# Optimization experiments

Hardware: AMD Instinct MI355X
Metric: run time of the kernel (lower is better)

The kernel has to match this reference:

```python
import jax, jax.numpy as jnp
import numpy as np

NUM_ENT, SEQ, H, OUT, NG = 10000, 10, 200, 100, 2048


def _seg_mean(x, idx, n):
    s = jax.ops.segment_sum(x, idx, num_segments=n)
    d = jax.ops.segment_sum(jnp.ones((idx.shape[0],), x.dtype), idx, num_segments=n)
    return s / jnp.maximum(d, 1.0)[:, None]


def setup_inputs() -> dict:
    k = jax.random.split(jax.random.key(0), 24)
    N, E, Nw, Ew, Vw, Rsel, MQ = 50000, 200000, 30000, 300000, 40000, 8192, 8
    f = lambda i, shp: jax.random.normal(k[i], shp, jnp.float32) * 0.05
    ri = lambda i, shp, hi: jax.random.randint(k[i], shp, 0, hi)
    return dict(
        ent_embeds=f(0, (NUM_ENT, H)), rel_embeds=f(1, (240, H)), word_embeds=f(2, (Vw, OUT)),
        gcn_w1=f(3, (OUT, H)), gcn_b1=jnp.zeros((H,), jnp.float32),
        gcn_w2=f(4, (H, H)), gcn_b2=jnp.zeros((H,), jnp.float32),
        cg1_wn=f(5, (H, OUT)), cg1_wl=f(6, (H, OUT)), cg1_wr=f(7, (H, OUT)),
        cg2_wn=f(8, (OUT, H)), cg2_wl=f(9, (OUT, H)), cg2_wr=f(10, (OUT, H)),
        attn_wa=f(11, (H, H)), attn_wc=f(12, (2 * H, H)),
        node_slot=jnp.arange(N), edge_src=ri(13, (E,), N), edge_dst=ri(14, (E,), N),
        edge_type=ri(15, (E,), 240), word_id=ri(16, (Nw,), Vw),
        wsrc=ri(17, (Ew,), Nw), wdst=ri(18, (Ew,), Nw),
        ent_word_idx=ri(19, (N, MQ), Nw), ent_word_mask=ri(20, (N, MQ), 2).astype(jnp.int32),
        rel_word_idx=ri(21, (Rsel, MQ), Nw), rel_word_mask=ri(22, (Rsel, MQ), 2).astype(jnp.int32),
        r_ids_graph=ri(23, (Rsel,), E), edge_slot=jnp.arange(Rsel))


def reference(ent_embeds, rel_embeds, word_embeds, gcn_w1, gcn_b1, gcn_w2, gcn_b2,
              cg1_wn, cg1_wl, cg1_wr, cg2_wn, cg2_wl, cg2_wr, attn_wa, attn_wc,
              node_slot, edge_src, edge_dst, edge_type, word_id, wsrc, wdst,
              ent_word_idx, ent_word_mask, rel_word_idx, rel_word_mask, r_ids_graph, edge_slot):
    N = node_slot.shape[0]
    Nw = word_id.shape[0]
    Rsel = r_ids_graph.shape[0]
    # --- se_aggr: 2-layer GCN over the batched word graph ---
    wh = word_embeds[word_id]                                   # [Nw,100]
    wh = jax.nn.relu(_seg_mean(wh[wsrc], wdst, Nw) @ gcn_w1 + gcn_b1)
    wh = jax.nn.relu(_seg_mean(wh[wsrc], wdst, Nw) @ gcn_w2 + gcn_b2)
    # --- re_aggr1/re_aggr2: CompGCN message passing on batched event graph ---
    h = ent_embeds[node_slot % NUM_ENT]                         # [N,200]
    e = rel_embeds[edge_type]                                   # [E,200]
    def compgcn(h, e, wn, wl, wr):
        agg = _seg_mean(h[edge_src] - e, edge_dst, N)           # sub-composition msgs
        return jax.nn.relu(agg @ wn + h @ wl), e @ wr
    h, e = compgcn(h, e, cg1_wn, cg1_wl, cg1_wr)                # 200 -> 100
    h, e = compgcn(h, e, cg2_wn, cg2_wl, cg2_wr)                # 100 -> 200
    embeds_g_r = e[r_ids_graph]                                 # [Rsel,200]
    # --- build Q_mx / H_mx (padded word-context groups) + 'general' attention ---
    Q = jnp.concatenate([h, embeds_g_r], 0)                     # [N+Rsel,200]
    H_ent = wh[ent_word_idx] * ent_word_mask[..., None].astype(wh.dtype)   # [N,8,200]
    H_rel = wh[rel_word_idx] * rel_word_mask[..., None].astype(wh.dtype)   # [Rsel,8,200]
    Hm = jnp.concatenate([H_ent, H_rel], 0)                     # [N+Rsel,8,200]
    scores = jnp.einsum('md,de,mke->mk', Q, attn_wa, Hm)
    attn = jax.nn.softmax(scores, axis=-1)
    ctx = jnp.einsum('mk,mkd->md', attn, Hm)
    out = jnp.tanh(jnp.concatenate([ctx, Q], -1) @ attn_wc)     # [N+Rsel,200]
    h_out, r_out = out[:N], out[N:]
    # --- temporal scatter of node embeddings per snapshot graph ---
    nid = node_slot % NUM_ENT
    gidx = node_slot // (N // SEQ)
    node_emb_temporal = jnp.zeros((NUM_ENT, SEQ, H), h_out.dtype).at[nid, gidx].set(h_out)
    # --- pack selected edge embeds into padded [NG, SEQ, H] sequence tensor ---
    per = Rsel // NG
    row, pos = edge_slot // per, edge_slot % per
    embed_seq = jnp.zeros((NG, SEQ, H), r_out.dtype).at[row, pos].set(r_out)
    return embed_seq, node_emb_temporal
```

## Files before the change

kernel.cpp:

```cpp
#include <hip/hip_runtime.h>
#include <cstddef>

constexpr int NUM_ENT_C = 10000;
constexpr int SEQ_C     = 10;
constexpr int H_C       = 200;
constexpr int OUT_C     = 100;
constexpr int NG_C      = 2048;
constexpr int NREL_C    = 240;
constexpr int MQ_C      = 8;

typedef __attribute__((ext_vector_type(8))) short          bf16x8;
typedef __attribute__((ext_vector_type(4))) float          f32x4;
typedef __attribute__((ext_vector_type(8))) unsigned short u16x8;

__device__ __forceinline__ unsigned short f2bf(float v) {
    unsigned u = __float_as_uint(v);
    unsigned r = (u + 0x7FFFu + ((u >> 16) & 1u)) >> 16;
    return (unsigned short)r;
}
__device__ __forceinline__ float bf2f(unsigned short b) {
    return __uint_as_float((unsigned)b << 16);
}
__device__ __forceinline__ void up2(unsigned u, float& lo, float& hi) {
    lo = __uint_as_float(u << 16);
    hi = __uint_as_float(u & 0xFFFF0000u);
}

__global__ void prep_k(const float* __restrict__ ent, unsigned short* __restrict__ entb, size_t e8,
                       const float* __restrict__ wemb, unsigned short* __restrict__ wembb, size_t w8,
                       int* __restrict__ wdeg, int Nw, int* __restrict__ edeg, int N) {
    size_t total = e8 + w8 + (size_t)Nw + (size_t)N;
    size_t stride = (size_t)gridDim.x * blockDim.x;
    for (size_t t = (size_t)blockIdx.x * blockDim.x + threadIdx.x; t < total; t += stride) {
        if (t < e8) {
            const float* s = ent + t * 8;
            u16x8 o;
            #pragma unroll
            for (int i = 0; i < 8; ++i) o[i] = f2bf(s[i]);
            *reinterpret_cast<u16x8*>(entb + t * 8) = o;
        } else if (t < e8 + w8) {
            size_t tt = t - e8;
            const float* s = wemb + tt * 8;
            u16x8 o;
            #pragma unroll
            for (int i = 0; i < 8; ++i) o[i] = f2bf(s[i]);
            *reinterpret_cast<u16x8*>(wembb + tt * 8) = o;
        } else if (t < e8 + w8 + (size_t)Nw) {
            wdeg[t - e8 - w8] = 0;
        } else {
            edeg[t - e8 - w8 - Nw] = 0;
        }
    }
}

__global__ void hist2_k(const int* __restrict__ wdst, int Ew, int* __restrict__ wdeg,
                        const int* __restrict__ edst, int E, int* __restrict__ edeg) {
    int total = Ew + E;
    int stride = gridDim.x * blockDim.x;
    for (int t = blockIdx.x * blockDim.x + threadIdx.x; t < total; t += stride) {
        if (t < Ew) atomicAdd(&wdeg[wdst[t]], 1);
        else        atomicAdd(&edeg[edst[t - Ew]], 1);
    }
}

__global__ void scanA_k(const int* __restrict__ v, int* __restrict__ bsum, int n) {
    __shared__ int s[256];
    int t = threadIdx.x;
    int i = blockIdx.x * 256 + t;
    s[t] = (i < n) ? v[i] : 0;
    __syncthreads();
    for (int d = 128; d; d >>= 1) {
        if (t < d) s[t] += s[t + d];
        __syncthreads();
    }
    if (t == 0) bsum[blockIdx.x] = s[0];
}

__global__ void scanB_k(int* __restrict__ bsum, int nb) {
    __shared__ int s[256];
    int t = threadIdx.x;
    int v = (t < nb) ? bsum[t] : 0;
    s[t] = v;
    __syncthreads();
    for (int d = 1; d < 256; d <<= 1) {
        int x = (t >= d) ? s[t - d] : 0;
        __syncthreads();
        s[t] += x;
        __syncthreads();
    }
    if (t < nb) bsum[t] = s[t] - v;
}

__global__ void scanC_k(const int* __restrict__ v, const int* __restrict__ bsum,
                        int* __restrict__ offs, int* __restrict__ cur, int n) {
    __shared__ int s[256];
    int t = threadIdx.x;
    int i = blockIdx.x * 256 + t;
    int val = (i < n) ? v[i] : 0;
    s[t] = val;
    __syncthreads();
    for (int d = 1; d < 256; d <<= 1) {
        int x = (t >= d) ? s[t - d] : 0;
        __syncthreads();
        s[t] += x;
        __syncthreads();
    }
    if (i < n) {
        int ex = s[t] - val + bsum[blockIdx.x];
        offs[i] = ex;
        cur[i]  = ex;
    }
}

__global__ void fill2_k(const int* __restrict__ wdst, const int* __restrict__ wsrc,
                        const int* __restrict__ word_id, int Ew,
                        int* __restrict__ wcur, int* __restrict__ wbktA, int* __restrict__ wbktB,
                        const int* __restrict__ edst, const int* __restrict__ esrc,
                        const int* __restrict__ etype, int E,
                        int* __restrict__ ecur, int* __restrict__ ebktS, int* __restrict__ ebktT) {
    int total = Ew + E;
    int stride = gridDim.x * blockDim.x;
    for (int t = blockIdx.x * blockDim.x + threadIdx.x; t < total; t += stride) {
        if (t < Ew) {
            int ws = wsrc[t];
            int p = atomicAdd(&wcur[wdst[t]], 1);
            wbktA[p] = word_id[ws];
            wbktB[p] = ws;
        } else {
            int e = t - Ew;
            int p = atomicAdd(&ecur[edst[e]], 1);
            ebktS[p] = esrc[e];
            ebktT[p] = etype[e];
        }
    }
}

template<int K1, int K2, int Kp, bool RELSUB, bool SRCMOD, bool SELFMOD, bool DUAL>
__global__ __launch_bounds__(256) void gather_mean_k(
        const unsigned short* __restrict__ feat, const unsigned short* __restrict__ selfT,
        const float* __restrict__ rel,
        const int* __restrict__ bktS, const int* __restrict__ bktT,
        const int* __restrict__ offs, const int* __restrict__ deg,
        unsigned short* __restrict__ dst, int n) {
    int node = blockIdx.x * 4 + (threadIdx.x >> 6);
    int lane = threadIdx.x & 63;
    if (node >= n) return;
    int off = offs[node], dg = deg[node];
    float acc[4] = {0.f, 0.f, 0.f, 0.f};
    unsigned short* drow = dst + (size_t)node * Kp;

    if (DUAL) {
        int half = lane >> 5, lh = lane & 31;
        int d0 = lh * 4;
        bool act = d0 < K1;
        for (int i = 0; i < dg; i += 2) {
            int ii = i + half;
            if (ii < dg && act) {
                int s = bktS[off + ii];
                if (SRCMOD) s = s % NUM_ENT_C;
                uint2 u = *reinterpret_cast<const uint2*>(feat + (size_t)s * K1 + d0);
                float e0, e1, e2, e3;
                up2(u.x, e0, e1); up2(u.y, e2, e3);
                if (RELSUB) {
                    int tt = bktT[off + ii];
                    float4 rv = *reinterpret_cast<const float4*>(rel + (size_t)tt * K1 + d0);
                    e0 -= rv.x; e1 -= rv.y; e2 -= rv.z; e3 -= rv.w;
                }
                acc[0] += e0; acc[1] += e1; acc[2] += e2; acc[3] += e3;
            }
        }
        #pragma unroll
        for (int c = 0; c < 4; ++c) acc[c] += __shfl_xor(acc[c], 32);
        float inv = 1.f / fmaxf((float)dg, 1.f);
        if (half == 0 && act) {
            uint2 o;
            o.x = (unsigned)f2bf(acc[0] * inv) | ((unsigned)f2bf(acc[1] * inv) << 16);
            o.y = (unsigned)f2bf(acc[2] * inv) | ((unsigned)f2bf(acc[3] * inv) << 16);
            *reinterpret_cast<uint2*>(drow + d0) = o;
        }
        if (K2 > 0 && half == 1 && d0 < K2) {
            int srow = SELFMOD ? (node % NUM_ENT_C) : node;
            uint2 sv = *reinterpret_cast<const uint2*>(selfT + (size_t)srow * K2 + d0);
            *reinterpret_cast<uint2*>(drow + K1 + d0) = sv;
        }
    } else {
        int d0 = lane * 4;
        bool act = d0 < K1;
        for (int i = 0; i < dg; ++i) {
            if (act) {
                int s = bktS[off + i];
                if (SRCMOD) s = s % NUM_ENT_C;
                uint2 u = *reinterpret_cast<const uint2*>(feat + (size_t)s * K1 + d0);
                float e0, e1, e2, e3;
                up2(u.x, e0, e1); up2(u.y, e2, e3);
                if (RELSUB) {
                    int tt = bktT[off + i];
                    float4 rv = *reinterpret_cast<const float4*>(rel + (size_t)tt * K1 + d0);
                    e0 -= rv.x; e1 -= rv.y; e2 -= rv.z; e3 -= rv.w;
                }
                acc[0] += e0; acc[1] += e1; acc[2] += e2; acc[3] += e3;
            }
        }
        float inv = 1.f / fmaxf((float)dg, 1.f);
        if (act) {
            uint2 o;
            o.x = (unsigned)f2bf(acc[0] * inv) | ((unsigned)f2bf(acc[1] * inv) << 16);
            o.y = (unsigned)f2bf(acc[2] * inv) | ((unsigned)f2bf(acc[3] * inv) << 16);
            *reinterpret_cast<uint2*>(drow + d0) = o;
        }
        if (K2 > 0 && d0 < K2) {
            int srow = SELFMOD ? (node % NUM_ENT_C) : node;
            uint2 sv = *reinterpret_cast<const uint2*>(selfT + (size_t)srow * K2 + d0);
            *reinterpret_cast<uint2*>(drow + K1 + d0) = sv;
        }
    }
    for (int cc = K1 + K2 + lane; cc < Kp; cc += 64) drow[cc] = 0;
}

__global__ void convw_all_k(const float* __restrict__ gcn_w1, const float* __restrict__ gcn_w2,
                            const float* __restrict__ cg1_wn, const float* __restrict__ cg1_wl,
                            const float* __restrict__ cg2_wn, const float* __restrict__ cg2_wl,
                            const float* __restrict__ attn_wa, const float* __restrict__ attn_wc,
                            unsigned short* __restrict__ Wt) {
    constexpr int S0 = 26624;
    constexpr int S1 = S0 + 46592;
    constexpr int S2 = S1 + 46592;
    constexpr int S3 = S2 + 46592;
    constexpr int S4 = S3 + 46592;
    constexpr int S5 = S4 + 86528;
    int stride = gridDim.x * blockDim.x;
    for (int t = blockIdx.x * blockDim.x + threadIdx.x; t < S5; t += stride) {
        float v = 0.f;
        if (t < S0) {
            int l = t, nn = l >> 7, k = l & 127;
            if (nn < 200 && k < 100) v = gcn_w1[k * 200 + nn];
        } else if (t < S1) {
            int l = t - S0, nn = l / 224, k = l - nn * 224;
            if (nn < 200 && k < 200) v = gcn_w2[k * 200 + nn];
        } else if (t < S2) {
            int l = t - S1, nn = l / 416, k = l - nn * 416;
            if (nn < 100) {
                if (k < 200)      v = cg1_wn[k * 100 + nn];
                else if (k < 400) v = cg1_wl[(k - 200) * 100 + nn];
            }
        } else if (t < S3) {
            int l = t - S2, nn = l / 224, k = l - nn * 224;
            if (nn < 200) {
                if (k < 100)      v = cg2_wn[k * 200 + nn];
                else if (k < 200) v = cg2_wl[(k - 100) * 200 + nn];
            }
        } else if (t < S4) {
            int l = t - S3, nn = l / 224, k = l - nn * 224;
            if (nn < 200 && k < 200) v = attn_wa[k * 200 + nn];
        } else {
            int l = t - S4, nn = l / 416, k = l - nn * 416;
            if (nn < 200 && k < 400) v = attn_wc[k * 200 + nn];
        }
        Wt[t] = f2bf(v);
    }
}

__global__ void post_k(const float* __restrict__ rel2, const int* __restrict__ edge_type,
                       const int* __restrict__ r_ids, unsigned short* __restrict__ A,
                       const int* __restrict__ node_slot, const int* __restrict__ edge_slot,
                       int* __restrict__ rowOff, int N, int M, int divq, int per, int embBase) {
    int R = M - N;
    size_t secA = (size_t)R * H_C;
    size_t secB = secA + (size_t)M * 6;
    size_t total = secB + (size_t)M;
    size_t stride = (size_t)gridDim.x * blockDim.x;
    for (size_t t = (size_t)blockIdx.x * blockDim.x + threadIdx.x; t < total; t += stride) {
        if (t < secA) {
            int r = (int)(t / H_C);
            int d = (int)(t - (size_t)r * H_C);
            int rr = r_ids[r];
            A[(size_t)(N + r) * 448 + 200 + d] = f2bf(rel2[(size_t)edge_type[rr] * H_C + d]);
        } else if (t < secB) {
            size_t l = t - secA;
            int m = (int)(l / 6), c = (int)(l - (size_t)m * 6);
            *reinterpret_cast<uint4*>(A + (size_t)m * 448 + 400 + c * 8) = make_uint4(0u, 0u, 0u, 0u);
        } else {
            int m = (int)(t - secB);
            int offv;
            if (m < N) {
                int ns = node_slot[m];
                offv = embBase + ((ns % NUM_ENT_C) * SEQ_C + ns / divq) * H_C;
            } else {
                int es = edge_slot[m - N];
                offv = ((es / per) * SEQ_C + (es - (es / per) * per)) * H_C;
            }
            rowOff[m] = offv;
        }
    }
}

template<int NF, int ACT, bool SCATTER, bool OBF16>
__global__ __launch_bounds__(256) void mfma_gemm_k(
        const unsigned short* __restrict__ A, int lda,
        const unsigned short* __restrict__ Wt,
        const float* __restrict__ bias, void* __restrict__ Cv, int ldc,
        const int* __restrict__ rowOff, int M, int N, int Kp) {
    constexpr int BN = NF * 16;
    __shared__ unsigned short As[128][40];
    __shared__ unsigned short Bs[BN][40];
    const int tid  = threadIdx.x;
    const int bm   = blockIdx.x * 128;
    const int w    = tid >> 6;
    const int lane = tid & 63;
    const int lr   = lane & 15;
    const int lk   = (lane >> 4) * 8;

    f32x4 acc0[NF], acc1[NF];
    #pragma unroll
    for (int nf = 0; nf < NF; ++nf) {
        acc0[nf] = (f32x4){0.f, 0.f, 0.f, 0.f};
        acc1[nf] = (f32x4){0.f, 0.f, 0.f, 0.f};
    }

    for (int k0 = 0; k0 < Kp; k0 += 32) {
        #pragma unroll
        for (int j = 0; j < 2; ++j) {
            int id = tid + j * 256;
            int m = id >> 2, c = id & 3;
            int gm = bm + m;
            uint4 v = make_uint4(0u, 0u, 0u, 0u);
            if (gm < M) v = *reinterpret_cast<const uint4*>(A + (size_t)gm * lda + k0 + c * 8);
            *reinterpret_cast<uint4*>(&As[m][c * 8]) = v;
        }
        for (int i = tid; i < NF * 64; i += 256) {
            int n = i >> 2, c = i & 3;
            uint4 v = *reinterpret_cast<const uint4*>(Wt + (size_t)n * Kp + k0 + c * 8);
            *reinterpret_cast<uint4*>(&Bs[n][c * 8]) = v;
        }
        __syncthreads();
        bf16x8 a0 = *reinterpret_cast<const bf16x8*>(&As[w * 16 + lr][lk]);
        bf16x8 a1 = *reinterpret_cast<const bf16x8*>(&As[64 + w * 16 + lr][lk]);
        #pragma unroll
        for (int nf = 0; nf < NF; ++nf) {
            bf16x8 b = *reinterpret_cast<const bf16x8*>(&Bs[nf * 16 + lr][lk]);
            acc0[nf] = __builtin_amdgcn_mfma_f32_16x16x32_bf16(a0, b, acc0[nf], 0, 0, 0);
            acc1[nf] = __builtin_amdgcn_mfma_f32_16x16x32_bf16(a1, b, acc1[nf], 0, 0, 0);
        }
        __syncthreads();
    }

    const int r0 = (lane >> 4) * 4;
    #pragma unroll
    for (int h = 0; h < 2; ++h) {
        #pragma unroll
        for (int j = 0; j < 4; ++j) {
            int gm = bm + h * 64 + w * 16 + r0 + j;
            if (gm >= M) continue;
            size_t base;
            if (SCATTER && !OBF16) base = (size_t)rowOff[gm];
            else                   base = (size_t)gm * ldc;
            #pragma unroll
            for (int nf = 0; nf < NF; ++nf) {
                int gn = nf * 16 + lr;
                if (gn >= N) continue;
                float v = h ? acc1[nf][j] : acc0[nf][j];
                if (bias) v += bias[gn];
                if (ACT == 1) v = fmaxf(v, 0.f);
                if (ACT == 2) v = tanhf(v);
                if (OBF16) ((unsigned short*)Cv)[base + gn] = f2bf(v);
                else       ((float*)Cv)[base + gn] = v;
            }
        }
    }
}

template<int NF, int ACT, bool SCATTER, bool OBF16>
static void launch_mfma(hipStream_t s, const unsigned short* A, int lda,
                        const unsigned short* Wt, const float* bias,
                        void* C, int ldc, const int* rowOff, int M, int N, int Kp) {
    mfma_gemm_k<NF, ACT, SCATTER, OBF16><<<dim3((M + 127) / 128), 256, 0, s>>>(
        A, lda, Wt, bias, C, ldc, rowOff, M, N, Kp);
}

__global__ __launch_bounds__(256) void gemm_f32_k(
        const float* __restrict__ A, const float* __restrict__ W,
        float* __restrict__ C, int M, int N, int K) {
    constexpr int TS = 64, BK = 16;
    __shared__ float As[BK][TS];
    __shared__ float Bs[BK][TS];
    int bm = blockIdx.x * TS, bn = blockIdx.y * TS;
    int tid = threadIdx.x;
    int tx = tid & 15, ty = tid >> 4;
    float acc[4][4] = {};
    for (int k0 = 0; k0 < K; k0 += BK) {
        #pragma unroll
        for (int l = tid; l < TS * BK; l += 256) {
            int m = l >> 4, kk = l & 15;
            int gm = bm + m, gk = k0 + kk;
            As[kk][m] = (gm < M && gk < K) ? A[(size_t)gm * K + gk] : 0.f;
        }
        #pragma unroll
        for (int l = tid; l < TS * BK; l += 256) {
            int kk = l >> 6, n = l & 63;
            int gk = k0 + kk, gn = bn + n;
            Bs[kk][n] = (gk < K && gn < N) ? W[(size_t)gk * N + gn] : 0.f;
        }
        __syncthreads();
        #pragma unroll
        for (int kk = 0; kk < BK; ++kk) {
            float a[4], b[4];
            #pragma unroll
            for (int i = 0; i < 4; ++i) a[i] = As[kk][ty * 4 + i];
            #pragma unroll
            for (int j = 0; j < 4; ++j) b[j] = Bs[kk][tx * 4 + j];
            #pragma unroll
            for (int i = 0; i < 4; ++i)
                #pragma unroll
                for (int j = 0; j < 4; ++j) acc[i][j] += a[i] * b[j];
        }
        __syncthreads();
    }
    #pragma unroll
    for (int i = 0; i < 4; ++i) {
        int gm = bm + ty * 4 + i;
        if (gm >= M) continue;
        #pragma unroll
        for (int j = 0; j < 4; ++j) {
            int gn = bn + tx * 4 + j;
            if (gn < N) C[(size_t)gm * N + gn] = acc[i][j];
        }
    }
}

__global__ __launch_bounds__(256) void attn_k(
        const unsigned short* __restrict__ QAb, const unsigned short* __restrict__ whb,
        const int* __restrict__ ent_idx, const int* __restrict__ ent_mask,
        const int* __restrict__ rel_idx, const int* __restrict__ rel_mask,
        unsigned short* __restrict__ ctxOut, int N, int M) {
    int m = blockIdx.x * 4 + (threadIdx.x >> 6);
    int lane = threadIdx.x & 63;
    if (m >= M) return;
    const int* idxp;
    const int* mskp;
    if (m < N) { idxp = ent_idx + (size_t)m * MQ_C;        mskp = ent_mask + (size_t)m * MQ_C; }
    else       { idxp = rel_idx + (size_t)(m - N) * MQ_C;  mskp = rel_mask + (size_t)(m - N) * MQ_C; }

    int d0 = lane * 4;
    bool act = d0 < H_C;
    float qa0 = 0.f, qa1 = 0.f, qa2 = 0.f, qa3 = 0.f;
    if (act) {
        uint2 u = *reinterpret_cast<const uint2*>(QAb + (size_t)m * H_C + d0);
        up2(u.x, qa0, qa1); up2(u.y, qa2, qa3);
    }
    int   idx[MQ_C];
    float msk[MQ_C];
    float s[MQ_C];
    uint2 wr[MQ_C];
    #pragma unroll
    for (int k = 0; k < MQ_C; ++k) { idx[k] = idxp[k]; msk[k] = (float)mskp[k]; }
    #pragma unroll
    for (int k = 0; k < MQ_C; ++k) {
        float p = 0.f;
        if (act) {
            wr[k] = *reinterpret_cast<const uint2*>(whb + (size_t)idx[k] * H_C + d0);
            float e0, e1, e2, e3;
            up2(wr[k].x, e0, e1); up2(wr[k].y, e2, e3);
            p = qa0 * e0 + qa1 * e1 + qa2 * e2 + qa3 * e3;
        } else {
            wr[k] = make_uint2(0u, 0u);
        }
        #pragma unroll
        for (int off = 32; off; off >>= 1) p += __shfl_xor(p, off);
        s[k] = p * msk[k];
    }
    float mx = s[0];
    #pragma unroll
    for (int k = 1; k < MQ_C; ++k) mx = fmaxf(mx, s[k]);
    float den = 0.f;
    #pragma unroll
    for (int k = 0; k < MQ_C; ++k) { s[k] = expf(s[k] - mx); den += s[k]; }
    float inv = 1.f / den;
    if (act) {
        float c0 = 0.f, c1 = 0.f, c2 = 0.f, c3 = 0.f;
        #pragma unroll
        for (int k = 0; k < MQ_C; ++k) {
            float a = s[k] * msk[k];
            float e0, e1, e2, e3;
            up2(wr[k].x, e0, e1); up2(wr[k].y, e2, e3);
            c0 += a * e0; c1 += a * e1; c2 += a * e2; c3 += a * e3;
        }
        uint2 o;
        o.x = (unsigned)f2bf(c0 * inv) | ((unsigned)f2bf(c1 * inv) << 16);
        o.y = (unsigned)f2bf(c2 * inv) | ((unsigned)f2bf(c3 * inv) << 16);
        *reinterpret_cast<uint2*>(ctxOut + (size_t)m * 448 + d0) = o;
    }
}


static inline dim3 ew_grid(size_t total) {
    size_t b = (total + 255) / 256;
    if (b > 4096) b = 4096;
    return dim3((unsigned)b);
}

extern "C" void kernel_launch(void* const* d_in, const int* in_sizes, int n_in,
                              void* d_out, int out_size, void* d_ws, size_t ws_size,
                              hipStream_t stream) {
    const float* ent_embeds = (const float*)d_in[0];
    const float* rel_embeds = (const float*)d_in[1];
    const float* word_embeds= (const float*)d_in[2];
    const float* gcn_w1     = (const float*)d_in[3];
    const float* gcn_b1     = (const float*)d_in[4];
    const float* gcn_w2     = (const float*)d_in[5];
    const float* gcn_b2     = (const float*)d_in[6];
    const float* cg1_wn     = (const float*)d_in[7];
    const float* cg1_wl     = (const float*)d_in[8];
    const float* cg1_wr     = (const float*)d_in[9];
    const float* cg2_wn     = (const float*)d_in[10];
    const float* cg2_wl     = (const float*)d_in[11];
    const float* cg2_wr     = (const float*)d_in[12];
    const float* attn_wa    = (const float*)d_in[13];
    const float* attn_wc    = (const float*)d_in[14];
    const int* node_slot    = (const int*)d_in[15];
    const int* edge_src     = (const int*)d_in[16];
    const int* edge_dst     = (const int*)d_in[17];
    const int* edge_type    = (const int*)d_in[18];
    const int* word_id      = (const int*)d_in[19];
    const int* wsrc         = (const int*)d_in[20];
    const int* wdst         = (const int*)d_in[21];
    const int* ent_word_idx = (const int*)d_in[22];
    const int* ent_word_mask= (const int*)d_in[23];
    const int* rel_word_idx = (const int*)d_in[24];
    const int* rel_word_mask= (const int*)d_in[25];
    const int* r_ids_graph  = (const int*)d_in[26];
    const int* edge_slot    = (const int*)d_in[27];

    const int N    = in_sizes[15];
    const int E    = in_sizes[16];
    const int Nw   = in_sizes[19];
    const int Ew   = in_sizes[20];
    const int Rsel = in_sizes[27];
    const int M    = N + Rsel;
    const int divq = N / SEQ_C;
    const int per  = Rsel / NG_C;
    const int embBase = NG_C * SEQ_C * H_C;
    const size_t entElems  = (size_t)in_sizes[0];
    const size_t wembElems = (size_t)in_sizes[2];

    float* ws = (float*)d_ws;
    size_t o = 0;
    auto align4 = [&]() { o = (o + 3) & ~(size_t)3; };
    int* wdeg  = (int*)(ws + o); o += Nw;
    int* woffs = (int*)(ws + o); o += Nw;
    int* wcur  = (int*)(ws + o); o += Nw;
    int* edeg  = (int*)(ws + o); o += N;
    int* eoffs = (int*)(ws + o); o += N;
    int* ecur  = (int*)(ws + o); o += N;
    int* wbktA = (int*)(ws + o); o += Ew;
    int* wbktB = (int*)(ws + o); o += Ew;
    int* ebktS = (int*)(ws + o); o += E;
    int* ebktT = (int*)(ws + o); o += E;
    int* bsum  = (int*)(ws + o); o += 256;
    int* rowOff= (int*)(ws + o); o += M;
    float* rel1 = ws + o; o += (size_t)NREL_C * OUT_C;
    float* rel2 = ws + o; o += (size_t)NREL_C * H_C;
    align4();
    unsigned short* Wt      = (unsigned short*)(ws + o); o += 299520 / 2;
    align4();
    unsigned short* wh_bf   = (unsigned short*)(ws + o); o += ((size_t)Nw * H_C) / 2;
    align4();
    unsigned short* h1_bf   = (unsigned short*)(ws + o); o += ((size_t)N * OUT_C) / 2;
    align4();
    unsigned short* ent_bf  = (unsigned short*)(ws + o); o += entElems / 2;
    align4();
    unsigned short* wemb_bf = (unsigned short*)(ws + o); o += wembElems / 2;
    align4();
    unsigned short* AbfF    = (unsigned short*)(ws + o); o += ((size_t)M * 448) / 2;
    align4();
    float* BIG = ws + o;
    unsigned short* wh1_bf = (unsigned short*)BIG;
    unsigned short* AbfW   = (unsigned short*)(BIG + ((size_t)Nw * H_C) / 2);
    unsigned short* AbfE   = (unsigned short*)BIG;
    unsigned short* QAb    = (unsigned short*)d_out;

    unsigned short* WT_g1 = Wt;
    unsigned short* WT_g2 = Wt + 26624;
    unsigned short* WT_c1 = Wt + 73216;
    unsigned short* WT_c2 = Wt + 119808;
    unsigned short* WT_wa = Wt + 166400;
    unsigned short* WT_wc = Wt + 212992;

    prep_k<<<ew_grid(entElems / 8 + wembElems / 8 + Nw + N), 256, 0, stream>>>(
        ent_embeds, ent_bf, entElems / 8, word_embeds, wemb_bf, wembElems / 8,
        wdeg, Nw, edeg, N);
    convw_all_k<<<ew_grid(299520), 256, 0, stream>>>(
        gcn_w1, gcn_w2, cg1_wn, cg1_wl, cg2_wn, cg2_wl, attn_wa, attn_wc, Wt);
    hist2_k<<<ew_grid((size_t)Ew + E), 256, 0, stream>>>(wdst, Ew, wdeg, edge_dst, E, edeg);
    {
        int nbW = (Nw + 255) / 256;
        scanA_k<<<nbW, 256, 0, stream>>>(wdeg, bsum, Nw);
        scanB_k<<<1, 256, 0, stream>>>(bsum, nbW);
        scanC_k<<<nbW, 256, 0, stream>>>(wdeg, bsum, woffs, wcur, Nw);
        int nbE = (N + 255) / 256;
        scanA_k<<<nbE, 256, 0, stream>>>(edeg, bsum, N);
        scanB_k<<<1, 256, 0, stream>>>(bsum, nbE);
        scanC_k<<<nbE, 256, 0, stream>>>(edeg, bsum, eoffs, ecur, N);
    }
    fill2_k<<<ew_grid((size_t)Ew + E), 256, 0, stream>>>(
        wdst, wsrc, word_id, Ew, wcur, wbktA, wbktB,
        edge_dst, edge_src, edge_type, E, ecur, ebktS, ebktT);
    gemm_f32_k<<<dim3((NREL_C + 63) / 64, (OUT_C + 63) / 64), 256, 0, stream>>>(
        rel_embeds, cg1_wr, rel1, NREL_C, OUT_C, H_C);
    gemm_f32_k<<<dim3((NREL_C + 63) / 64, (H_C + 63) / 64), 256, 0, stream>>>(
        rel1, cg2_wr, rel2, NREL_C, H_C, OUT_C);
    post_k<<<ew_grid((size_t)Rsel * H_C + (size_t)M * 7), 256, 0, stream>>>(
        rel2, edge_type, r_ids_graph, AbfF, node_slot, edge_slot, rowOff,
        N, M, divq, per, embBase);

    gather_mean_k<OUT_C, 0, 128, false, false, false, true><<<dim3((Nw + 3) / 4), 256, 0, stream>>>(
        wemb_bf, nullptr, nullptr, wbktA, nullptr, woffs, wdeg, AbfW, Nw);
    launch_mfma<13, 1, false, true>(stream, AbfW, 128, WT_g1, gcn_b1, wh1_bf, H_C, nullptr, Nw, H_C, 128);
    gather_mean_k<H_C, 0, 224, false, false, false, false><<<dim3((Nw + 3) / 4), 256, 0, stream>>>(
        wh1_bf, nullptr, nullptr, wbktB, nullptr, woffs, wdeg, AbfW, Nw);
    launch_mfma<13, 1, false, true>(stream, AbfW, 224, WT_g2, gcn_b2, wh_bf, H_C, nullptr, Nw, H_C, 224);

    gather_mean_k<H_C, H_C, 448, true, true, true, false><<<dim3((N + 3) / 4), 256, 0, stream>>>(
        ent_bf, ent_bf, rel_embeds, ebktS, ebktT, eoffs, edeg, AbfE, N);
    launch_mfma<7, 1, false, true>(stream, AbfE, 448, WT_c1, nullptr, h1_bf, OUT_C, nullptr, N, OUT_C, 416);
    gather_mean_k<OUT_C, OUT_C, 224, true, false, false, true><<<dim3((N + 3) / 4), 256, 0, stream>>>(
        h1_bf, h1_bf, rel1, ebktS, ebktT, eoffs, edeg, AbfE, N);
    launch_mfma<13, 1, false, true>(stream, AbfE, 224, WT_c2, nullptr, AbfF + 200, 448, nullptr, N, H_C, 224);

    launch_mfma<13, 0, false, true>(stream, AbfF + 200, 448, WT_wa, nullptr, QAb, H_C, nullptr, M, H_C, 224);
    attn_k<<<(M + 3) / 4, 256, 0, stream>>>(QAb, wh_bf, ent_word_idx, ent_word_mask,
                                            rel_word_idx, rel_word_mask, AbfF, N, M);
    hipMemsetAsync(d_out, 0, (size_t)out_size * 4, stream);
    launch_mfma<13, 2, true, false>(stream, AbfF, 448, WT_wc, nullptr, d_out, H_C, rowOff, M, H_C, 416);
}
```

Before: 722.9 us.

## Merge word and entity CSR builds into one scan; unroll gathers; skip masked attention loads

The word-graph and event-graph degree arrays and buckets now share one concatenated CSR, so a single three-kernel scan replaces two. This removes three kernel launches and their serialization, and scanB grows to 512 threads to cover the larger block count. The non-dual gather loop is unrolled by two to keep more independent loads in flight. The attention kernel skips loading and reducing word rows whose mask is zero, which saves memory traffic but adds a divergent branch.

```diff
diff --git a/kernel.cpp b/kernel.cpp
--- a/kernel.cpp
+++ b/kernel.cpp
@@ -28,8 +28,8 @@
 
 __global__ void prep_k(const float* __restrict__ ent, unsigned short* __restrict__ entb, size_t e8,
                        const float* __restrict__ wemb, unsigned short* __restrict__ wembb, size_t w8,
-                       int* __restrict__ wdeg, int Nw, int* __restrict__ edeg, int N) {
-    size_t total = e8 + w8 + (size_t)Nw + (size_t)N;
+                       int* __restrict__ cdeg, int nNodes) {
+    size_t total = e8 + w8 + (size_t)nNodes;
     size_t stride = (size_t)gridDim.x * blockDim.x;
     for (size_t t = (size_t)blockIdx.x * blockDim.x + threadIdx.x; t < total; t += stride) {
         if (t < e8) {
@@ -45,21 +45,20 @@
             #pragma unroll
             for (int i = 0; i < 8; ++i) o[i] = f2bf(s[i]);
             *reinterpret_cast<u16x8*>(wembb + tt * 8) = o;
-        } else if (t < e8 + w8 + (size_t)Nw) {
-            wdeg[t - e8 - w8] = 0;
         } else {
-            edeg[t - e8 - w8 - Nw] = 0;
-        }
-    }
-}
-
-__global__ void hist2_k(const int* __restrict__ wdst, int Ew, int* __restrict__ wdeg,
-                        const int* __restrict__ edst, int E, int* __restrict__ edeg) {
+            cdeg[t - e8 - w8] = 0;
+        }
+    }
+}
+
+__global__ void hist2_k(const int* __restrict__ wdst, int Ew,
+                        const int* __restrict__ edst, int E,
+                        int* __restrict__ cdeg, int Nw) {
     int total = Ew + E;
     int stride = gridDim.x * blockDim.x;
     for (int t = blockIdx.x * blockDim.x + threadIdx.x; t < total; t += stride) {
-        if (t < Ew) atomicAdd(&wdeg[wdst[t]], 1);
-        else        atomicAdd(&edeg[edst[t - Ew]], 1);
+        if (t < Ew) atomicAdd(&cdeg[wdst[t]], 1);
+        else        atomicAdd(&cdeg[Nw + edst[t - Ew]], 1);
     }
 }
 
@@ -77,12 +76,12 @@
 }
 
 __global__ void scanB_k(int* __restrict__ bsum, int nb) {
-    __shared__ int s[256];
+    __shared__ int s[512];
     int t = threadIdx.x;
     int v = (t < nb) ? bsum[t] : 0;
     s[t] = v;
     __syncthreads();
-    for (int d = 1; d < 256; d <<= 1) {
+    for (int d = 1; d < 512; d <<= 1) {
         int x = (t >= d) ? s[t - d] : 0;
         __syncthreads();
         s[t] += x;
@@ -114,23 +113,23 @@
 
 __global__ void fill2_k(const int* __restrict__ wdst, const int* __restrict__ wsrc,
                         const int* __restrict__ word_id, int Ew,
-                        int* __restrict__ wcur, int* __restrict__ wbktA, int* __restrict__ wbktB,
                         const int* __restrict__ edst, const int* __restrict__ esrc,
                         const int* __restrict__ etype, int E,
-                        int* __restrict__ ecur, int* __restrict__ ebktS, int* __restrict__ ebktT) {
+                        int* __restrict__ ccur, int Nw,
+                        int* __restrict__ bktA, int* __restrict__ bktB) {
     int total = Ew + E;
     int stride = gridDim.x * blockDim.x;
     for (int t = blockIdx.x * blockDim.x + threadIdx.x; t < total; t += stride) {
         if (t < Ew) {
-            int ws = wsrc[t];
-            int p = atomicAdd(&wcur[wdst[t]], 1);
-            wbktA[p] = word_id[ws];
-            wbktB[p] = ws;
+            int s = wsrc[t];
+            int p = atomicAdd(&ccur[wdst[t]], 1);
+            bktA[p] = word_id[s];
+            bktB[p] = s;
         } else {
             int e = t - Ew;
-            int p = atomicAdd(&ecur[edst[e]], 1);
-            ebktS[p] = esrc[e];
-            ebktT[p] = etype[e];
+            int p = atomicAdd(&ccur[Nw + edst[e]], 1);
+            bktA[p] = esrc[e];
+            bktB[p] = etype[e];
         }
     }
 }
@@ -186,11 +185,31 @@
     } else {
         int d0 = lane * 4;
         bool act = d0 < K1;
-        for (int i = 0; i < dg; ++i) {
+        int i = 0;
+        for (; i + 2 <= dg; i += 2) {
+            int s0 = bktS[off + i], s1 = bktS[off + i + 1];
+            if (SRCMOD) { s0 = s0 % NUM_ENT_C; s1 = s1 % NUM_ENT_C; }
             if (act) {
-                int s = bktS[off + i];
-                if (SRCMOD) s = s % NUM_ENT_C;
-                uint2 u = *reinterpret_cast<const uint2*>(feat + (size_t)s * K1 + d0);
+                uint2 u0 = *reinterpret_cast<const uint2*>(feat + (size_t)s0 * K1 + d0);
+                uint2 u1 = *reinterpret_cast<const uint2*>(feat + (size_t)s1 * K1 + d0);
+                float a0, a1, a2, a3, b0, b1, b2, b3;
+                up2(u0.x, a0, a1); up2(u0.y, a2, a3);
+                up2(u1.x, b0, b1); up2(u1.y, b2, b3);
+                if (RELSUB) {
+                    int t0 = bktT[off + i], t1 = bktT[off + i + 1];
+                    float4 r0 = *reinterpret_cast<const float4*>(rel + (size_t)t0 * K1 + d0);
+                    float4 r1 = *reinterpret_cast<const float4*>(rel + (size_t)t1 * K1 + d0);
+                    a0 -= r0.x; a1 -= r0.y; a2 -= r0.z; a3 -= r0.w;
+                    b0 -= r1.x; b1 -= r1.y; b2 -= r1.z; b3 -= r1.w;
+                }
+                acc[0] += a0 + b0; acc[1] += a1 + b1; acc[2] += a2 + b2; acc[3] += a3 + b3;
+            }
+        }
+        if (i < dg) {
+            int s0 = bktS[off + i];
+            if (SRCMOD) s0 = s0 % NUM_ENT_C;
+            if (act) {
+                uint2 u = *reinterpret_cast<const uint2*>(feat + (size_t)s0 * K1 + d0);
                 float e0, e1, e2, e3;
                 up2(u.x, e0, e1); up2(u.y, e2, e3);
                 if (RELSUB) {
@@ -447,26 +466,31 @@
         uint2 u = *reinterpret_cast<const uint2*>(QAb + (size_t)m * H_C + d0);
         up2(u.x, qa0, qa1); up2(u.y, qa2, qa3);
     }
-    int   idx[MQ_C];
-    float msk[MQ_C];
+    int  idx[MQ_C];
+    int  msk[MQ_C];
     float s[MQ_C];
     uint2 wr[MQ_C];
     #pragma unroll
-    for (int k = 0; k < MQ_C; ++k) { idx[k] = idxp[k]; msk[k] = (float)mskp[k]; }
+    for (int k = 0; k < MQ_C; ++k) { idx[k] = idxp[k]; msk[k] = mskp[k]; }
     #pragma unroll
     for (int k = 0; k < MQ_C; ++k) {
-        float p = 0.f;
-        if (act) {
-            wr[k] = *reinterpret_cast<const uint2*>(whb + (size_t)idx[k] * H_C + d0);
-            float e0, e1, e2, e3;
-            up2(wr[k].x, e0, e1); up2(wr[k].y, e2, e3);
-            p = qa0 * e0 + qa1 * e1 + qa2 * e2 + qa3 * e3;
+        if (msk[k] != 0) {
+            float p = 0.f;
+            if (act) {
+                wr[k] = *reinterpret_cast<const uint2*>(whb + (size_t)idx[k] * H_C + d0);
+                float e0, e1, e2, e3;
+                up2(wr[k].x, e0, e1); up2(wr[k].y, e2, e3);
+                p = qa0 * e0 + qa1 * e1 + qa2 * e2 + qa3 * e3;
+            } else {
+                wr[k] = make_uint2(0u, 0u);
+            }
+            #pragma unroll
+            for (int off = 32; off; off >>= 1) p += __shfl_xor(p, off);
+            s[k] = p;
         } else {
+            s[k] = 0.f;
             wr[k] = make_uint2(0u, 0u);
         }
-        #pragma unroll
-        for (int off = 32; off; off >>= 1) p += __shfl_xor(p, off);
-        s[k] = p * msk[k];
     }
     float mx = s[0];
     #pragma unroll
@@ -479,10 +503,11 @@
         float c0 = 0.f, c1 = 0.f, c2 = 0.f, c3 = 0.f;
         #pragma unroll
         for (int k = 0; k < MQ_C; ++k) {
-            float a = s[k] * msk[k];
-            float e0, e1, e2, e3;
-            up2(wr[k].x, e0, e1); up2(wr[k].y, e2, e3);
-            c0 += a * e0; c1 += a * e1; c2 += a * e2; c3 += a * e3;
+            if (msk[k] != 0) {
+                float e0, e1, e2, e3;
+                up2(wr[k].x, e0, e1); up2(wr[k].y, e2, e3);
+                c0 += s[k] * e0; c1 += s[k] * e1; c2 += s[k] * e2; c3 += s[k] * e3;
+            }
         }
         uint2 o;
         o.x = (unsigned)f2bf(c0 * inv) | ((unsigned)f2bf(c1 * inv) << 16);
@@ -541,21 +566,17 @@
     const int embBase = NG_C * SEQ_C * H_C;
     const size_t entElems  = (size_t)in_sizes[0];
     const size_t wembElems = (size_t)in_sizes[2];
+    const int nNodes = Nw + N;
 
     float* ws = (float*)d_ws;
     size_t o = 0;
     auto align4 = [&]() { o = (o + 3) & ~(size_t)3; };
-    int* wdeg  = (int*)(ws + o); o += Nw;
-    int* woffs = (int*)(ws + o); o += Nw;
-    int* wcur  = (int*)(ws + o); o += Nw;
-    int* edeg  = (int*)(ws + o); o += N;
-    int* eoffs = (int*)(ws + o); o += N;
-    int* ecur  = (int*)(ws + o); o += N;
-    int* wbktA = (int*)(ws + o); o += Ew;
-    int* wbktB = (int*)(ws + o); o += Ew;
-    int* ebktS = (int*)(ws + o); o += E;
-    int* ebktT = (int*)(ws + o); o += E;
-    int* bsum  = (int*)(ws + o); o += 256;
+    int* cdeg  = (int*)(ws + o); o += nNodes;
+    int* coffs = (int*)(ws + o); o += nNodes;
+    int* ccur  = (int*)(ws + o); o += nNodes;
+    int* bktA  = (int*)(ws + o); o += Ew + E;
+    int* bktB  = (int*)(ws + o); o += Ew + E;
+    int* bsum  = (int*)(ws + o); o += 512;
     int* rowOff= (int*)(ws + o); o += M;
     float* rel1 = ws + o; o += (size_t)NREL_C * OUT_C;
     float* rel2 = ws + o; o += (size_t)NREL_C * H_C;
@@ -585,25 +606,20 @@
     unsigned short* WT_wa = Wt + 166400;
     unsigned short* WT_wc = Wt + 212992;
 
-    prep_k<<<ew_grid(entElems / 8 + wembElems / 8 + Nw + N), 256, 0, stream>>>(
+    prep_k<<<ew_grid(entElems / 8 + wembElems / 8 + nNodes), 256, 0, stream>>>(
         ent_embeds, ent_bf, entElems / 8, word_embeds, wemb_bf, wembElems / 8,
-        wdeg, Nw, edeg, N);
+        cdeg, nNodes);
     convw_all_k<<<ew_grid(299520), 256, 0, stream>>>(
         gcn_w1, gcn_w2, cg1_wn, cg1_wl, cg2_wn, cg2_wl, attn_wa, attn_wc, Wt);
-    hist2_k<<<ew_grid((size_t)Ew + E), 256, 0, stream>>>(wdst, Ew, wdeg, edge_dst, E, edeg);
+    hist2_k<<<ew_grid((size_t)Ew + E), 256, 0, stream>>>(wdst, Ew, edge_dst, E, cdeg, Nw);
     {
-        int nbW = (Nw + 255) / 256;
-        scanA_k<<<nbW, 256, 0, stream>>>(wdeg, bsum, Nw);
-        scanB_k<<<1, 256, 0, stream>>>(bsum, nbW);
-        scanC_k<<<nbW, 256, 0, stream>>>(wdeg, bsum, woffs, wcur, Nw);
-        int nbE = (N + 255) / 256;
-        scanA_k<<<nbE, 256, 0, stream>>>(edeg, bsum, N);
-        scanB_k<<<1, 256, 0, stream>>>(bsum, nbE);
-        scanC_k<<<nbE, 256, 0, stream>>>(edeg, bsum, eoffs, ecur, N);
+        int nb = (nNodes + 255) / 256;
+        scanA_k<<<nb, 256, 0, stream>>>(cdeg, bsum, nNodes);
+        scanB_k<<<1, 512, 0, stream>>>(bsum, nb);
+        scanC_k<<<nb, 256, 0, stream>>>(cdeg, bsum, coffs, ccur, nNodes);
     }
     fill2_k<<<ew_grid((size_t)Ew + E), 256, 0, stream>>>(
-        wdst, wsrc, word_id, Ew, wcur, wbktA, wbktB,
-        edge_dst, edge_src, edge_type, E, ecur, ebktS, ebktT);
+        wdst, wsrc, word_id, Ew, edge_dst, edge_src, edge_type, E, ccur, Nw, bktA, bktB);
     gemm_f32_k<<<dim3((NREL_C + 63) / 64, (OUT_C + 63) / 64), 256, 0, stream>>>(
         rel_embeds, cg1_wr, rel1, NREL_C, OUT_C, H_C);
     gemm_f32_k<<<dim3((NREL_C + 63) / 64, (H_C + 63) / 64), 256, 0, stream>>>(
@@ -613,17 +629,17 @@
         N, M, divq, per, embBase);
 
     gather_mean_k<OUT_C, 0, 128, false, false, false, true><<<dim3((Nw + 3) / 4), 256, 0, stream>>>(
-        wemb_bf, nullptr, nullptr, wbktA, nullptr, woffs, wdeg, AbfW, Nw);
+        wemb_bf, nullptr, nullptr, bktA, nullptr, coffs, cdeg, AbfW, Nw);
     launch_mfma<13, 1, false, true>(stream, AbfW, 128, WT_g1, gcn_b1, wh1_bf, H_C, nullptr, Nw, H_C, 128);
     gather_mean_k<H_C, 0, 224, false, false, false, false><<<dim3((Nw + 3) / 4), 256, 0, stream>>>(
-        wh1_bf, nullptr, nullptr, wbktB, nullptr, woffs, wdeg, AbfW, Nw);
+        wh1_bf, nullptr, nullptr, bktB, nullptr, coffs, cdeg, AbfW, Nw);
     launch_mfma<13, 1, false, true>(stream, AbfW, 224, WT_g2, gcn_b2, wh_bf, H_C, nullptr, Nw, H_C, 224);
 
     gather_mean_k<H_C, H_C, 448, true, true, true, false><<<dim3((N + 3) / 4), 256, 0, stream>>>(
-        ent_bf, ent_bf, rel_embeds, ebktS, ebktT, eoffs, edeg, AbfE, N);
+        ent_bf, ent_bf, rel_embeds, bktA, bktB, coffs + Nw, cdeg + Nw, AbfE, N);
     launch_mfma<7, 1, false, true>(stream, AbfE, 448, WT_c1, nullptr, h1_bf, OUT_C, nullptr, N, OUT_C, 416);
     gather_mean_k<OUT_C, OUT_C, 224, true, false, false, true><<<dim3((N + 3) / 4), 256, 0, stream>>>(
-        h1_bf, h1_bf, rel1, ebktS, ebktT, eoffs, edeg, AbfE, N);
+        h1_bf, h1_bf, rel1, bktA, bktB, coffs + Nw, cdeg + Nw, AbfE, N);
     launch_mfma<13, 1, false, true>(stream, AbfE, 224, WT_c2, nullptr, AbfF + 200, 448, nullptr, N, H_C, 224);
 
     launch_mfma<13, 0, false, true>(stream, AbfF + 200, 448, WT_wa, nullptr, QAb, H_C, nullptr, M, H_C, 224);
```

After: 818.9 us. 13.3% more time.
